# Optimization experiments

Hardware: AMD Instinct MI355X
Metric: run time of the kernel (lower is better)

The kernel has to match this reference:

```python
import jax, jax.numpy as jnp
import numpy as np

B = 32768   # batch (agents)
H = 64      # h_dim
E = 16      # embedding_dim
M = 6       # num_modes (n_samples)
P = M * 2   # traj_points
T = 30      # pred_len (seq_len)


def setup_inputs() -> dict:
    key = jax.random.key(0)
    ks = jax.random.split(key, 14)
    def s(k, shape, scale=0.1):
        return jax.random.normal(k, shape, jnp.float32) * scale
    return dict(
        traj_abs=s(ks[0], (1, B, 2), 1.0),
        traj_rel=s(ks[1], (1, B, 2), 1.0),
        h0=s(ks[2], (1, B, H)),
        c0=s(ks[3], (1, B, H)),
        W_ih=s(ks[4], (4 * H, E)),
        W_hh=s(ks[5], (4 * H, H)),
        b_ih=s(ks[6], (4 * H,)),
        b_hh=s(ks[7], (4 * H,)),
        W_se=s(ks[8], (E, P)),
        b_se=s(ks[9], (E,)),
        W_pos=s(ks[10], (P, H)),
        b_pos=s(ks[11], (P,)),
        W_conf=s(ks[12], (M, H)),
        b_conf=s(ks[13], (M,)),
    )


def reference(traj_abs, traj_rel, h0, c0, W_ih, W_hh, b_ih, b_hh,
              W_se, b_se, W_pos, b_pos, W_conf, b_conf):
    b = traj_rel.shape[1]
    # repeat_interleave the (x,y) pair num_modes times along feature dim -> [b, 12]
    rel12 = jnp.tile(traj_rel.reshape(b, 1, 2), (1, M, 1)).reshape(b, P)
    x = jax.nn.leaky_relu(rel12 @ W_se.T + b_se)  # [b, E]
    h = h0[0]
    c = c0[0]

    def step(carry, _):
        x, h, c = carry
        # PyTorch LSTM cell, gate order i, f, g, o
        gates = x @ W_ih.T + b_ih + h @ W_hh.T + b_hh  # [b, 4H]
        i, f, g, o = jnp.split(gates, 4, axis=-1)
        c = jax.nn.sigmoid(f) * c + jax.nn.sigmoid(i) * jnp.tanh(g)
        h = jax.nn.sigmoid(o) * jnp.tanh(c)
        rel = h @ W_pos.T + b_pos                      # [b, P]
        x = jax.nn.leaky_relu(rel @ W_se.T + b_se)     # [b, E]
        return (x, h, c), rel

    (x, h, c), rels = jax.lax.scan(step, (x, h, c), None, length=T)  # rels: [T, b, P]
    pred = rels.reshape(T, b, M, 2).transpose(1, 2, 0, 3)            # [b, M, T, 2]
    conf = jax.nn.softmax(h @ W_conf.T + b_conf, axis=1)             # [b, M]
    return pred, conf
```

## Files before the change

kernel.cpp:

```cpp
#include <hip/hip_runtime.h>
#include <hip/hip_bf16.h>

typedef _Float16 half8 __attribute__((ext_vector_type(8)));
typedef _Float16 half4 __attribute__((ext_vector_type(4)));
typedef float float4v __attribute__((ext_vector_type(4)));

#define BATCH 32768
#define TT 30

#if __has_builtin(__builtin_amdgcn_exp2f)
#define FEXP2(x) __builtin_amdgcn_exp2f(x)
#else
#define FEXP2(x) __expf((x) * 0.6931471805599453f)
#endif
#if __has_builtin(__builtin_amdgcn_rcpf)
#define FRCP(x) __builtin_amdgcn_rcpf(x)
#else
#define FRCP(x) (1.0f / (x))
#endif

#define NLOG2E  -1.4426950408889634f
#define N2LOG2E -2.8853900817779268f

#define WFRAG_OFF 0
#define WCF_OFF   12288
#define BIASB_OFF 13312
#define SXY_OFF   13568
#define CBIAS_OFF 13616
#define WCONF_OFF 13648
#define BCONF_OFF 14032
#define FLAG_IDX  14038
#define CONF_BASE (BATCH * 360)

__global__ void detect_kernel(const unsigned short* __restrict__ raw,
                              int* __restrict__ flag_out) {
    __shared__ int sflag[256];
    int local = 0;
    for (int i = threadIdx.x; i < 16384; i += 256) {
        unsigned short u = raw[i];
        if ((u & 0x7F80u) == 0x7F80u) local = 1;
    }
    sflag[threadIdx.x] = local;
    __syncthreads();
    if (threadIdx.x == 0) {
        int f = 0;
        for (int i = 0; i < 256; ++i) f |= sflag[i];
        flag_out[0] = f;
    }
}

__device__ __forceinline__ float ldin(const void* p, int i, int isf32) {
    return isf32 ? ((const float*)p)[i]
                 : (float)((const __hip_bfloat16*)p)[i];
}

__global__ void prep_kernel(const void* __restrict__ W_ih,
                            const void* __restrict__ W_hh,
                            const void* __restrict__ b_ih,
                            const void* __restrict__ b_hh,
                            const void* __restrict__ W_se,
                            const void* __restrict__ b_se,
                            const void* __restrict__ W_pos,
                            const void* __restrict__ b_pos,
                            const void* __restrict__ W_conf,
                            const void* __restrict__ b_conf,
                            float* __restrict__ ws)
{
    const int isf32 = ((const int*)(ws + FLAG_IDX))[0];
    int tid = blockIdx.x * blockDim.x + threadIdx.x;
    int stride = gridDim.x * blockDim.x;
    _Float16* wfh = (_Float16*)ws;

    for (int idx = tid; idx < 24576; idx += stride) {
        int jj = idx & 7, r = idx >> 3;
        int lane = r & 63; r >>= 6;
        int ks = r % 3; r /= 3;
        int tl = r & 7; int uhh = r >> 3;
        int col = lane & 15, akq = lane >> 4;
        int k = ks * 32 + akq * 8 + jj;
        int gate = tl >> 1, us = tl & 1;
        int row = gate * 64 + uhh * 32 + us * 16 + col;
        float v = 0.f;
        if (k < 16) v = ldin(W_ih, row * 16 + k, isf32);
        else if (k < 80) v = ldin(W_hh, row * 64 + (k - 16), isf32);
        v *= (gate == 2) ? N2LOG2E : NLOG2E;
        wfh[idx] = (_Float16)v;
    }
    _Float16* wch = (_Float16*)(ws + WCF_OFF);
    for (int idx = tid; idx < 2048; idx += stride) {
        int jj = idx & 7, r = idx >> 3;
        int lane = r & 63; r >>= 6;
        int ks = r & 1, uhh = r >> 1;
        int col = lane & 15, akq = lane >> 4;
        int k = ks * 32 + akq * 8 + jj;
        float v = 0.f;
        if (uhh == 0) {
            if (col < 12) v = ldin(W_pos, col * 64 + k, isf32);
        } else {
            float s = 0.f;
            for (int p = 0; p < 12; ++p)
                s += ldin(W_se, col * 12 + p, isf32) * ldin(W_pos, p * 64 + k, isf32);
            v = s;
        }
        wch[idx] = (_Float16)v;
    }
    for (int idx = tid; idx < 256; idx += stride) {
        int gate = idx >> 6;
        float scale = (gate == 2) ? N2LOG2E : NLOG2E;
        ws[BIASB_OFF + idx] = (ldin(b_ih, idx, isf32) + ldin(b_hh, idx, isf32)) * scale;
    }
    for (int idx = tid; idx < 16; idx += stride) {
        float sx = 0.f, sy = 0.f;
        for (int m = 0; m < 6; ++m) {
            sx += ldin(W_se, idx * 12 + 2 * m, isf32);
            sy += ldin(W_se, idx * 12 + 2 * m + 1, isf32);
        }
        ws[SXY_OFF + idx * 3 + 0] = sx;
        ws[SXY_OFF + idx * 3 + 1] = sy;
        ws[SXY_OFF + idx * 3 + 2] = ldin(b_se, idx, isf32);
    }
    for (int idx = tid; idx < 32; idx += stride) {
        int w = idx >> 4, cc = idx & 15;
        float v = 0.f;
        if (w == 0) {
            if (cc < 12) v = ldin(b_pos, cc, isf32);
        } else {
            float s = ldin(b_se, cc, isf32);
            for (int p = 0; p < 12; ++p)
                s += ldin(W_se, cc * 12 + p, isf32) * ldin(b_pos, p, isf32);
            v = s;
        }
        ws[CBIAS_OFF + idx] = v;
    }
    for (int idx = tid; idx < 384; idx += stride)
        ws[WCONF_OFF + idx] = ldin(W_conf, idx, isf32);
    for (int idx = tid; idx < 6; idx += stride)
        ws[BCONF_OFF + idx] = ldin(b_conf, idx, isf32);
}

__global__ __launch_bounds__(128, 2) void lstm_kernel(
    const void* __restrict__ traj_rel,
    const void* __restrict__ h0,
    const void* __restrict__ c0,
    const float* __restrict__ ws,
    float* __restrict__ out)
{
    __shared__ _Float16 zsh[2 * 16 * 104];
    __shared__ _Float16 predh[12 * 30 * 36];

    const int tid = threadIdx.x;
    const int lane = tid & 63;
    const int uh = __builtin_amdgcn_readfirstlane(tid >> 6);
    const int col16 = lane & 15;
    const int akq = lane >> 4;
    const int base = blockIdx.x * 32;
    const int isf32 = ((const int*)(ws + FLAG_IDX))[0];

    const float4v* wfg = (const float4v*)ws;
    half8 Bf[8][3];
#pragma unroll
    for (int tl = 0; tl < 8; ++tl)
#pragma unroll
        for (int ks = 0; ks < 3; ++ks)
            Bf[tl][ks] = __builtin_bit_cast(half8,
                wfg[((uh * 8 + tl) * 3 + ks) * 64 + lane]);
    float bias8[8];
#pragma unroll
    for (int tl = 0; tl < 8; ++tl)
        bias8[tl] = ws[BIASB_OFF + (tl >> 1) * 64 + uh * 32 + (tl & 1) * 16 + col16];
    half8 wfc[2];
    {
        const float4v* wcg = (const float4v*)(ws + WCF_OFF);
#pragma unroll
        for (int ks = 0; ks < 2; ++ks)
            wfc[ks] = __builtin_bit_cast(half8, wcg[(uh * 2 + ks) * 64 + lane]);
    }
    const float cb = ws[CBIAS_OFF + uh * 16 + col16];

    float cg0[8], cg1[8];
#pragma unroll
    for (int us = 0; us < 2; ++us)
#pragma unroll
        for (int i = 0; i < 4; ++i) {
            int unit = uh * 32 + us * 16 + col16;
            cg0[us * 4 + i] = ldin(c0, (base + akq * 4 + i) * 64 + unit, isf32);
            cg1[us * 4 + i] = ldin(c0, (base + 16 + akq * 4 + i) * 64 + unit, isf32);
        }
    {
        int m = tid & 31, jq = tid >> 5;
        int g = m >> 4, row = m & 15;
        _Float16* zg = &zsh[g * 1664];
        half8 ha, hb;
#pragma unroll
        for (int i = 0; i < 8; ++i)
            ha[i] = (_Float16)ldin(h0, (base + m) * 64 + jq * 16 + i, isf32);
#pragma unroll
        for (int i = 0; i < 8; ++i)
            hb[i] = (_Float16)ldin(h0, (base + m) * 64 + jq * 16 + 8 + i, isf32);
        *(half8*)&zg[row * 104 + 16 + jq * 16] = ha;
        *(half8*)&zg[row * 104 + 16 + jq * 16 + 8] = hb;
        float rx = ldin(traj_rel, 2 * (base + m), isf32);
        float ry = ldin(traj_rel, 2 * (base + m) + 1, isf32);
        half4 xs;
#pragma unroll
        for (int i = 0; i < 4; ++i) {
            int e = 4 * jq + i;
            float x = fmaf(rx, ws[SXY_OFF + e * 3],
                      fmaf(ry, ws[SXY_OFF + e * 3 + 1], ws[SXY_OFF + e * 3 + 2]));
            xs[i] = (_Float16)(x > 0.f ? x : 0.01f * x);
        }
        *(half4*)&zg[row * 104 + 4 * jq] = xs;
        if (jq == 0) {
            half8 zz = {};
            *(half8*)&zg[row * 104 + 80] = zz;
            *(half8*)&zg[row * 104 + 88] = zz;
        }
    }
    __syncthreads();

    const int zbA = col16 * 104 + akq * 8;
    const int zbC = zbA + 16;
    const int hwb = 16 + uh * 32 + col16;

    float4v acc0[8], acc1[8];

#define ZG(g) (&zsh[(g) * 1664])

#define PHASE_A(G, ACC) do {                                                  \
    _Float16* zg_ = ZG(G);                                                    \
    _Pragma("unroll")                                                         \
    for (int tl = 0; tl < 8; ++tl) {                                          \
        float bv = bias8[tl];                                                 \
        ACC[tl][0] = bv; ACC[tl][1] = bv; ACC[tl][2] = bv; ACC[tl][3] = bv;   \
    }                                                                         \
    _Pragma("unroll")                                                         \
    for (int ks = 0; ks < 3; ++ks) {                                          \
        half8 af_ = *(const half8*)&zg_[zbA + ks * 32];                       \
        _Pragma("unroll")                                                     \
        for (int tl = 0; tl < 8; ++tl)                                        \
            ACC[tl] = __builtin_amdgcn_mfma_f32_16x16x32_f16(                 \
                af_, Bf[tl][ks], ACC[tl], 0, 0, 0);                           \
    }                                                                         \
} while (0)

#define PHASE_B(G, ACC, CARR) do {                                            \
    _Float16* zg_ = ZG(G);                                                    \
    _Pragma("unroll")                                                         \
    for (int us = 0; us < 2; ++us) {                                          \
        _Pragma("unroll")                                                     \
        for (int i = 0; i < 4; ++i) {                                         \
            float si = FRCP(1.0f + FEXP2(ACC[us][i]));                        \
            float sf = FRCP(1.0f + FEXP2(ACC[2 + us][i]));                    \
            float tg = fmaf(2.0f, FRCP(1.0f + FEXP2(ACC[4 + us][i])), -1.0f); \
            float so = FRCP(1.0f + FEXP2(ACC[6 + us][i]));                    \
            float cn = fmaf(sf, CARR[us * 4 + i], si * tg);                   \
            CARR[us * 4 + i] = cn;                                            \
            float th = fmaf(2.0f, FRCP(1.0f + FEXP2(cn * N2LOG2E)), -1.0f);   \
            float hn = so * th;                                               \
            zg_[(akq * 4 + i) * 104 + hwb + us * 16] = (_Float16)hn;          \
        }                                                                     \
    }                                                                         \
} while (0)


#define PHASE_C(G, T) do {                                                    \
    _Float16* zg_ = ZG(G);                                                    \
    float4v racc_;                                                            \
    racc_[0] = cb; racc_[1] = cb; racc_[2] = cb; racc_[3] = cb;               \
    _Pragma("unroll")                                                         \
    for (int ks = 0; ks < 2; ++ks) {                                          \
        half8 af_ = *(const half8*)&zg_[zbC + ks * 32];                       \
        racc_ = __builtin_amdgcn_mfma_f32_16x16x32_f16(                       \
            af_, wfc[ks], racc_, 0, 0, 0);                                    \
    }                                                                         \
    if (uh == 0) {                                                            \
        if (col16 < 12) {                                                     \
            half4 hv_;                                                        \
            _Pragma("unroll")                                                 \
            for (int i = 0; i < 4; ++i) hv_[i] = (_Float16)racc_[i];          \
            *(half4*)&predh[(col16 * 30 + (T)) * 36 + (G) * 16 + akq * 4] = hv_; \
        }                                                                     \
    } else if ((T) != TT - 1) {                                               \
        _Pragma("unroll")                                                     \
        for (int i = 0; i < 4; ++i) {                                         \
            float xv_ = racc_[i];                                             \
            xv_ = xv_ > 0.f ? xv_ : 0.01f * xv_;                              \
            zg_[(akq * 4 + i) * 104 + col16] = (_Float16)xv_;                 \
        }                                                                     \
    }                                                                         \
} while (0)

    PHASE_A(0, acc0);
    __syncthreads();
    PHASE_A(1, acc1); PHASE_B(0, acc0, cg0);
    __syncthreads();
    PHASE_C(0, 0);    PHASE_B(1, acc1, cg1);
    __syncthreads();

    for (int t = 1; t < TT; ++t) {
        PHASE_A(0, acc0); PHASE_C(1, t - 1);
        __syncthreads();
        PHASE_A(1, acc1); PHASE_B(0, acc0, cg0);
        __syncthreads();
        PHASE_C(0, t);    PHASE_B(1, acc1, cg1);
        __syncthreads();
    }
    PHASE_C(1, TT - 1);
    __syncthreads();

    {
        float4* po4 = (float4*)(out + (size_t)base * 360);
#pragma unroll 1
        for (int q2 = 0; q2 < 23; ++q2) {
            int idx4 = q2 * 128 + tid;
            if (idx4 < 2880) {
                int a = idx4 / 90, rem = idx4 % 90;
                int m = rem / 15, tq = rem % 15;
                int t0 = tq * 2;
                float4 o;
                o.x = (float)predh[((2 * m + 0) * 30 + t0) * 36 + a];
                o.y = (float)predh[((2 * m + 1) * 30 + t0) * 36 + a];
                o.z = (float)predh[((2 * m + 0) * 30 + t0 + 1) * 36 + a];
                o.w = (float)predh[((2 * m + 1) * 30 + t0 + 1) * 36 + a];
                po4[idx4] = o;
            }
        }
    }

    if (uh == 0 && lane < 32) {
        int m = lane;
        int g = m >> 4, row = m & 15;
        float l[6];
#pragma unroll
        for (int md = 0; md < 6; ++md) l[md] = ws[BCONF_OFF + md];
        for (int jj = 0; jj < 64; ++jj) {
            float hv = (float)zsh[g * 1664 + row * 104 + 16 + jj];
#pragma unroll
            for (int md = 0; md < 6; ++md)
                l[md] = fmaf(hv, ws[WCONF_OFF + md * 64 + jj], l[md]);
        }
        float mx = l[0];
#pragma unroll
        for (int md = 1; md < 6; ++md) mx = fmaxf(mx, l[md]);
        float ex[6], s = 0.f;
#pragma unroll
        for (int md = 0; md < 6; ++md) { ex[md] = __expf(l[md] - mx); s += ex[md]; }
        float inv = FRCP(s);
#pragma unroll
        for (int md = 0; md < 6; ++md)
            out[CONF_BASE + (size_t)(base + m) * 6 + md] = ex[md] * inv;
    }
}

extern "C" void kernel_launch(void* const* d_in, const int* in_sizes, int n_in,
                              void* d_out, int out_size, void* d_ws, size_t ws_size,
                              hipStream_t stream) {
    const void* traj_rel = d_in[1];
    const void* h0   = d_in[2];
    const void* c0   = d_in[3];
    const void* W_ih = d_in[4];
    const void* W_hh = d_in[5];
    const void* b_ih = d_in[6];
    const void* b_hh = d_in[7];
    const void* W_se = d_in[8];
    const void* b_se = d_in[9];
    const void* W_pos  = d_in[10];
    const void* b_pos  = d_in[11];
    const void* W_conf = d_in[12];
    const void* b_conf = d_in[13];
    float* ws = (float*)d_ws;
    float* out = (float*)d_out;

    detect_kernel<<<1, 256, 0, stream>>>((const unsigned short*)W_hh,
                                         (int*)(ws + FLAG_IDX));
    prep_kernel<<<40, 256, 0, stream>>>(W_ih, W_hh, b_ih, b_hh, W_se, b_se,
                                        W_pos, b_pos, W_conf, b_conf, ws);
    lstm_kernel<<<BATCH / 32, 128, 0, stream>>>(traj_rel, h0, c0, ws, out);
}
```

Measured before the change: 208.5 us.

## Split LSTM gate work across four waves per block instead of two

```diff
diff --git a/kernel.cpp b/kernel.cpp
--- a/kernel.cpp
+++ b/kernel.cpp
@@ -75,11 +75,10 @@
         int jj = idx & 7, r = idx >> 3;
         int lane = r & 63; r >>= 6;
         int ks = r % 3; r /= 3;
-        int tl = r & 7; int uhh = r >> 3;
+        int gate = r & 3; int wv = r >> 2;
         int col = lane & 15, akq = lane >> 4;
         int k = ks * 32 + akq * 8 + jj;
-        int gate = tl >> 1, us = tl & 1;
-        int row = gate * 64 + uhh * 32 + us * 16 + col;
+        int row = gate * 64 + wv * 16 + col;
         float v = 0.f;
         if (k < 16) v = ldin(W_ih, row * 16 + k, isf32);
         else if (k < 80) v = ldin(W_hh, row * 64 + (k - 16), isf32);
@@ -90,11 +89,11 @@
     for (int idx = tid; idx < 2048; idx += stride) {
         int jj = idx & 7, r = idx >> 3;
         int lane = r & 63; r >>= 6;
-        int ks = r & 1, uhh = r >> 1;
+        int ks = r & 1, role = r >> 1;
         int col = lane & 15, akq = lane >> 4;
         int k = ks * 32 + akq * 8 + jj;
         float v = 0.f;
-        if (uhh == 0) {
+        if (role == 0) {
             if (col < 12) v = ldin(W_pos, col * 64 + k, isf32);
         } else {
             float s = 0.f;
@@ -138,7 +137,7 @@
         ws[BCONF_OFF + idx] = ldin(b_conf, idx, isf32);
 }
 
-__global__ __launch_bounds__(128, 2) void lstm_kernel(
+__global__ __launch_bounds__(256, 4) void lstm_kernel(
     const void* __restrict__ traj_rel,
     const void* __restrict__ h0,
     const void* __restrict__ c0,
@@ -150,94 +149,91 @@
 
     const int tid = threadIdx.x;
     const int lane = tid & 63;
-    const int uh = __builtin_amdgcn_readfirstlane(tid >> 6);
+    const int wid = __builtin_amdgcn_readfirstlane(tid >> 6);
+    const int role = wid & 1;
     const int col16 = lane & 15;
     const int akq = lane >> 4;
     const int base = blockIdx.x * 32;
     const int isf32 = ((const int*)(ws + FLAG_IDX))[0];
 
     const float4v* wfg = (const float4v*)ws;
-    half8 Bf[8][3];
-#pragma unroll
-    for (int tl = 0; tl < 8; ++tl)
+    half8 Bf[4][3];
+#pragma unroll
+    for (int tl = 0; tl < 4; ++tl)
 #pragma unroll
         for (int ks = 0; ks < 3; ++ks)
             Bf[tl][ks] = __builtin_bit_cast(half8,
-                wfg[((uh * 8 + tl) * 3 + ks) * 64 + lane]);
-    float bias8[8];
-#pragma unroll
-    for (int tl = 0; tl < 8; ++tl)
-        bias8[tl] = ws[BIASB_OFF + (tl >> 1) * 64 + uh * 32 + (tl & 1) * 16 + col16];
+                wfg[((wid * 4 + tl) * 3 + ks) * 64 + lane]);
+    float bias4[4];
+#pragma unroll
+    for (int tl = 0; tl < 4; ++tl)
+        bias4[tl] = ws[BIASB_OFF + tl * 64 + wid * 16 + col16];
     half8 wfc[2];
     {
         const float4v* wcg = (const float4v*)(ws + WCF_OFF);
 #pragma unroll
         for (int ks = 0; ks < 2; ++ks)
-            wfc[ks] = __builtin_bit_cast(half8, wcg[(uh * 2 + ks) * 64 + lane]);
-    }
-    const float cb = ws[CBIAS_OFF + uh * 16 + col16];
-
-    float cg0[8], cg1[8];
-#pragma unroll
-    for (int us = 0; us < 2; ++us)
+            wfc[ks] = __builtin_bit_cast(half8, wcg[(role * 2 + ks) * 64 + lane]);
+    }
+    const float cb = ws[CBIAS_OFF + role * 16 + col16];
+
+    float cg0[4], cg1[4];
+    {
+        int unit = wid * 16 + col16;
 #pragma unroll
         for (int i = 0; i < 4; ++i) {
-            int unit = uh * 32 + us * 16 + col16;
-            cg0[us * 4 + i] = ldin(c0, (base + akq * 4 + i) * 64 + unit, isf32);
-            cg1[us * 4 + i] = ldin(c0, (base + 16 + akq * 4 + i) * 64 + unit, isf32);
-        }
+            cg0[i] = ldin(c0, (base + akq * 4 + i) * 64 + unit, isf32);
+            cg1[i] = ldin(c0, (base + 16 + akq * 4 + i) * 64 + unit, isf32);
+        }
+    }
     {
-        int m = tid & 31, jq = tid >> 5;
+        int m = tid & 31, jq2 = tid >> 5;
         int g = m >> 4, row = m & 15;
         _Float16* zg = &zsh[g * 1664];
-        half8 ha, hb;
+        half8 ha;
 #pragma unroll
         for (int i = 0; i < 8; ++i)
-            ha[i] = (_Float16)ldin(h0, (base + m) * 64 + jq * 16 + i, isf32);
-#pragma unroll
-        for (int i = 0; i < 8; ++i)
-            hb[i] = (_Float16)ldin(h0, (base + m) * 64 + jq * 16 + 8 + i, isf32);
-        *(half8*)&zg[row * 104 + 16 + jq * 16] = ha;
-        *(half8*)&zg[row * 104 + 16 + jq * 16 + 8] = hb;
-        float rx = ldin(traj_rel, 2 * (base + m), isf32);
-        float ry = ldin(traj_rel, 2 * (base + m) + 1, isf32);
-        half4 xs;
-#pragma unroll
-        for (int i = 0; i < 4; ++i) {
-            int e = 4 * jq + i;
-            float x = fmaf(rx, ws[SXY_OFF + e * 3],
-                      fmaf(ry, ws[SXY_OFF + e * 3 + 1], ws[SXY_OFF + e * 3 + 2]));
-            xs[i] = (_Float16)(x > 0.f ? x : 0.01f * x);
-        }
-        *(half4*)&zg[row * 104 + 4 * jq] = xs;
-        if (jq == 0) {
+            ha[i] = (_Float16)ldin(h0, (base + m) * 64 + jq2 * 8 + i, isf32);
+        *(half8*)&zg[row * 104 + 16 + jq2 * 8] = ha;
+        if (jq2 < 4) {
+            float rx = ldin(traj_rel, 2 * (base + m), isf32);
+            float ry = ldin(traj_rel, 2 * (base + m) + 1, isf32);
+            half4 xs;
+#pragma unroll
+            for (int i = 0; i < 4; ++i) {
+                int e = 4 * jq2 + i;
+                float x = fmaf(rx, ws[SXY_OFF + e * 3],
+                          fmaf(ry, ws[SXY_OFF + e * 3 + 1], ws[SXY_OFF + e * 3 + 2]));
+                xs[i] = (_Float16)(x > 0.f ? x : 0.01f * x);
+            }
+            *(half4*)&zg[row * 104 + 4 * jq2] = xs;
+        } else if (jq2 < 6) {
             half8 zz = {};
-            *(half8*)&zg[row * 104 + 80] = zz;
-            *(half8*)&zg[row * 104 + 88] = zz;
+            *(half8*)&zg[row * 104 + 80 + (jq2 - 4) * 8] = zz;
         }
     }
     __syncthreads();
 
     const int zbA = col16 * 104 + akq * 8;
     const int zbC = zbA + 16;
-    const int hwb = 16 + uh * 32 + col16;
-
-    float4v acc0[8], acc1[8];
+    const int hwb = 16 + wid * 16 + col16;
+
+    float4v acc0[4], acc1[4];
 
 #define ZG(g) (&zsh[(g) * 1664])
 
 #define PHASE_A(G, ACC) do {                                                  \
     _Float16* zg_ = ZG(G);                                                    \
     _Pragma("unroll")                                                         \
-    for (int tl = 0; tl < 8; ++tl) {                                          \
-        float bv = bias8[tl];                                                 \
+    for (int tl = 0; tl < 4; ++tl) {                                          \
+        float bv = bias4[tl];                                                 \
         ACC[tl][0] = bv; ACC[tl][1] = bv; ACC[tl][2] = bv; ACC[tl][3] = bv;   \
     }                                                                         \
     _Pragma("unroll")                                                         \
     for (int ks = 0; ks < 3; ++ks) {                                          \
         half8 af_ = *(const half8*)&zg_[zbA + ks * 32];                       \
         _Pragma("unroll")                                                     \
-        for (int tl = 0; tl < 8; ++tl)                                        \
+        for (int tl = 0; tl < 4; ++tl)                                        \
             ACC[tl] = __builtin_amdgcn_mfma_f32_16x16x32_f16(                 \
                 af_, Bf[tl][ks], ACC[tl], 0, 0, 0);                           \
     }                                                                         \
@@ -246,22 +242,18 @@
 #define PHASE_B(G, ACC, CARR) do {                                            \
     _Float16* zg_ = ZG(G);                                                    \
     _Pragma("unroll")                                                         \
-    for (int us = 0; us < 2; ++us) {                                          \
-        _Pragma("unroll")                                                     \
-        for (int i = 0; i < 4; ++i) {                                         \
-            float si = FRCP(1.0f + FEXP2(ACC[us][i]));                        \
-            float sf = FRCP(1.0f + FEXP2(ACC[2 + us][i]));                    \
-            float tg = fmaf(2.0f, FRCP(1.0f + FEXP2(ACC[4 + us][i])), -1.0f); \
-            float so = FRCP(1.0f + FEXP2(ACC[6 + us][i]));                    \
-            float cn = fmaf(sf, CARR[us * 4 + i], si * tg);                   \
-            CARR[us * 4 + i] = cn;                                            \
-            float th = fmaf(2.0f, FRCP(1.0f + FEXP2(cn * N2LOG2E)), -1.0f);   \
-            float hn = so * th;                                               \
-            zg_[(akq * 4 + i) * 104 + hwb + us * 16] = (_Float16)hn;          \
-        }                                                                     \
+    for (int i = 0; i < 4; ++i) {                                             \
+        float si = FRCP(1.0f + FEXP2(ACC[0][i]));                             \
+        float sf = FRCP(1.0f + FEXP2(ACC[1][i]));                             \
+        float tg = fmaf(2.0f, FRCP(1.0f + FEXP2(ACC[2][i])), -1.0f);          \
+        float so = FRCP(1.0f + FEXP2(ACC[3][i]));                             \
+        float cn = fmaf(sf, CARR[i], si * tg);                                \
+        CARR[i] = cn;                                                         \
+        float th = fmaf(2.0f, FRCP(1.0f + FEXP2(cn * N2LOG2E)), -1.0f);       \
+        float hn = so * th;                                                   \
+        zg_[(akq * 4 + i) * 104 + hwb] = (_Float16)hn;                        \
     }                                                                         \
 } while (0)
-
 
 #define PHASE_C(G, T) do {                                                    \
     _Float16* zg_ = ZG(G);                                                    \
@@ -273,7 +265,7 @@
         racc_ = __builtin_amdgcn_mfma_f32_16x16x32_f16(                       \
             af_, wfc[ks], racc_, 0, 0, 0);                                    \
     }                                                                         \
-    if (uh == 0) {                                                            \
+    if (role == 0) {                                                          \
         if (col16 < 12) {                                                     \
             half4 hv_;                                                        \
             _Pragma("unroll")                                                 \
@@ -294,25 +286,28 @@
     __syncthreads();
     PHASE_A(1, acc1); PHASE_B(0, acc0, cg0);
     __syncthreads();
-    PHASE_C(0, 0);    PHASE_B(1, acc1, cg1);
+    if (wid < 2) PHASE_C(0, 0);
+    PHASE_B(1, acc1, cg1);
     __syncthreads();
 
     for (int t = 1; t < TT; ++t) {
-        PHASE_A(0, acc0); PHASE_C(1, t - 1);
+        PHASE_A(0, acc0);
+        if (wid >= 2) PHASE_C(1, t - 1);
         __syncthreads();
         PHASE_A(1, acc1); PHASE_B(0, acc0, cg0);
         __syncthreads();
-        PHASE_C(0, t);    PHASE_B(1, acc1, cg1);
+        if (wid < 2) PHASE_C(0, t);
+        PHASE_B(1, acc1, cg1);
         __syncthreads();
     }
-    PHASE_C(1, TT - 1);
+    if (wid >= 2) PHASE_C(1, TT - 1);
     __syncthreads();
 
     {
         float4* po4 = (float4*)(out + (size_t)base * 360);
 #pragma unroll 1
-        for (int q2 = 0; q2 < 23; ++q2) {
-            int idx4 = q2 * 128 + tid;
+        for (int q2 = 0; q2 < 12; ++q2) {
+            int idx4 = q2 * 256 + tid;
             if (idx4 < 2880) {
                 int a = idx4 / 90, rem = idx4 % 90;
                 int m = rem / 15, tq = rem % 15;
@@ -327,7 +322,7 @@
         }
     }
 
-    if (uh == 0 && lane < 32) {
+    if (wid == 0 && lane < 32) {
         int m = lane;
         int g = m >> 4, row = m & 15;
         float l[6];
@@ -375,5 +370,5 @@
                                          (int*)(ws + FLAG_IDX));
     prep_kernel<<<40, 256, 0, stream>>>(W_ih, W_hh, b_ih, b_hh, W_se, b_se,
                                         W_pos, b_pos, W_conf, b_conf, ws);
-    lstm_kernel<<<BATCH / 32, 128, 0, stream>>>(traj_rel, h0, c0, ws, out);
-}
+    lstm_kernel<<<BATCH / 32, 256, 0, stream>>>(traj_rel, h0, c0, ws, out);
+}
```

After: 207.9 us. Within noise of the previous version (-0.3%).
